# Optimization experiments

Hardware: AMD Instinct MI355X
Metric: run time of the kernel (lower is better)

The kernel has to match this reference:

```python
import jax, jax.numpy as jnp
import numpy as np

CASCADES = 3
D, H, W = 64, 256, 256
HID = 8  # BasicBlock hidden channels


def fdiff(x, axis):
    """Forward difference D x along `axis` (last entry 0) == sparse dx/dy/dz matmul."""
    axis = axis % x.ndim
    pad = [(0, 0)] * x.ndim
    pad[axis] = (0, 1)
    return jnp.pad(jnp.diff(x, axis=axis), pad)


def fdiff_t(y, axis):
    """Exact transpose D^T y of fdiff: (D^T y)_0=-y_0, (D^T y)_j=y_{j-1}-y_j, (D^T y)_{n-1}=y_{n-2}."""
    axis = axis % y.ndim
    n = y.shape[axis]
    yl = jax.lax.slice_in_dim(y, 0, n - 1, axis=axis)  # y[0..n-2]
    pf = [(0, 0)] * y.ndim; pf[axis] = (1, 0)
    pb = [(0, 0)] * y.ndim; pb[axis] = (0, 1)
    return jnp.pad(yl, pf) - jnp.pad(yl, pb)


def conv3d(x, w, b):
    out = jax.lax.conv_general_dilated(
        x, w, window_strides=(1, 1, 1), padding='SAME',
        dimension_numbers=('NCDHW', 'OIDHW', 'NCDHW'))
    return out + b[None, :, None, None, None]


def basic_block(x, w1, b1, w2, b2):
    h = jax.nn.relu(conv3d(x, w1, b1))
    return conv3d(h, w2, b2), jnp.mean(jnp.abs(h))


def ite(t, sino):
    """BeijingGeometry stand-in: one SIRT-style step A^T(sino - A t)/D, A = sum over depth."""
    proj = jnp.sum(t, axis=2)               # [B,1,H,W]
    res = sino - proj
    return jnp.broadcast_to(res[:, :, None], t.shape) / t.shape[2]


def setup_inputs() -> dict:
    key = jax.random.key(0)
    ks = jax.random.split(key, 8)
    image = jax.random.normal(ks[0], (1, 1, D, H, W), dtype=jnp.float32)
    sino = jax.random.normal(ks[1], (1, 1, H, W), dtype=jnp.float32)
    # 4 BasicBlocks stacked on leading axis
    W1 = jax.random.normal(ks[2], (4, HID, 1, 3, 3, 3), dtype=jnp.float32) * 0.1
    B1 = jnp.zeros((4, HID), dtype=jnp.float32)
    W2 = jax.random.normal(ks[3], (4, 1, HID, 3, 3, 3), dtype=jnp.float32) * 0.1
    B2 = jnp.zeros((4, 1), dtype=jnp.float32)
    ntx = jnp.full((CASCADES,), -0.01, dtype=jnp.float32)
    nty = jnp.full((CASCADES,), -0.01, dtype=jnp.float32)
    ntz = jnp.full((CASCADES,), -0.01, dtype=jnp.float32)
    nt = jnp.full((CASCADES,), -0.1, dtype=jnp.float32)
    return {"image": image, "sino": sino, "W1": W1, "B1": B1, "W2": W2, "B2": B2,
            "ntx": ntx, "nty": nty, "ntz": ntz, "nt": nt}


def reference(image, sino, W1, B1, W2, B2, ntx, nty, ntz, nt):
    t = image
    p = q = s = jnp.float32(0.0)
    outs = [image]
    for c in range(CASCADES):
        z = t + ite(t, sino)
        pnew, _ = basic_block(fdiff(z, -1), W1[0], B1[0], W2[0], B2[0])  # d/dx (W axis)
        qnew, _ = basic_block(fdiff(z, -2), W1[1], B1[1], W2[1], B2[1])  # d/dy (H axis)
        snew, _ = basic_block(fdiff(z, -3), W1[2], B1[2], W2[2], B2[2])  # d/dz (D axis)
        znew, _ = basic_block(z, W1[3], B1[3], W2[3], B2[3])
        p = p + ntx[c] * (p - pnew)
        q = q + nty[c] * (q - qnew)
        s = s + ntz[c] * (s - snew)
        z_ = t + nt[c] * (t - znew)
        t = fdiff_t(p, -1) + fdiff_t(q, -2) + fdiff_t(s, -3) + z_
        outs.append(t)
    return jnp.stack(outs, axis=0)  # [cascades+1, B, 1, D, H, W]
```

## Files before the change

kernel.cpp:

```cpp
#include <hip/hip_runtime.h>

#define DD 64
#define HH 256
#define WW 256
#define HW (HH * WW)
#define NVOX (DD * HW)

#define TS 32
#define DR 36
#define HR 34
#define HP 34
#define CHB 22

__global__ __launch_bounds__(256) void k_corr(const float* __restrict__ t,
                                              const float* __restrict__ sino,
                                              float* __restrict__ corr) {
  int idx = blockIdx.x * 256 + threadIdx.x;
  float s = 0.f;
#pragma unroll 8
  for (int d = 0; d < DD; ++d) s += t[d * HW + idx];
  corr[idx] = (sino[idx] - s) * (1.0f / DD);
}

__global__ __launch_bounds__(256, 3) void k_blocks(
    const float* __restrict__ t, const float* __restrict__ corr,
    float* __restrict__ p, float* __restrict__ q, float* __restrict__ s_,
    float* __restrict__ zb,
    const float* __restrict__ W1g, const float* __restrict__ B1g,
    const float* __restrict__ W2g, const float* __restrict__ B2g,
    const float* __restrict__ ntx, const float* __restrict__ nty,
    const float* __restrict__ ntz, const float* __restrict__ nt, int c) {
  __shared__ __align__(16) float dbuf[3][DR][DR];
  __shared__ __align__(16) float hbuf[8][HR][HP];

  const int b = blockIdx.z & 3;
  const int D0 = (blockIdx.z >> 2) * CHB;
  const int Dend = (D0 + CHB < DD) ? (D0 + CHB) : DD;
  const int ty0 = blockIdx.y * TS;
  const int tx0 = blockIdx.x * TS;
  const int tid = threadIdx.x;

  const float* w1 = W1g + b * 216;
  const float* w2 = W2g + b * 216;
  const float b2 = B2g[b];
  const float coef = (b == 0) ? ntx[c] : (b == 1) ? nty[c] : (b == 2) ? ntz[c] : nt[c];
  const float* prevBuf = (b == 0) ? p : (b == 1) ? q : (b == 2) ? s_ : t;
  float* outBuf = (b == 0) ? p : (b == 1) ? q : (b == 2) ? s_ : zb;
  const bool zeroPrev = (c == 0) && (b < 3);

  auto dslot = [](int f) { return (f + 6) % 3; };

  auto load_deriv = [&](int f) {
    int sl = dslot(f);
    for (int i = tid; i < DR * DR; i += 256) {
      int iy = i / DR, ix = i - iy * DR;
      int gy = ty0 - 2 + iy, gx = tx0 - 2 + ix;
      float v = 0.f;
      if (f >= 0 && f < DD && (unsigned)gy < HH && (unsigned)gx < WW) {
        int base = f * HW + gy * WW + gx;
        int cb = gy * WW + gx;
        if (b == 0) {
          if (gx + 1 < WW) v = t[base + 1] - t[base] + corr[cb + 1] - corr[cb];
        } else if (b == 1) {
          if (gy + 1 < HH) v = t[base + WW] - t[base] + corr[cb + WW] - corr[cb];
        } else if (b == 2) {
          if (f + 1 < DD) v = t[base + HW] - t[base];
        } else {
          v = t[base] + corr[cb];
        }
      }
      dbuf[sl][iy][ix] = v;
    }
  };

  auto comp_hidden = [&](int e) {
    const float* d0 = &dbuf[dslot(e - 1)][0][0];
    const float* d1 = &dbuf[dslot(e)][0][0];
    const float* d2 = &dbuf[dslot(e + 1)][0][0];
    for (int pi = tid; pi < 17 * 17; pi += 256) {
      int pr = pi / 17, pc = pi - pr * 17;
      int jy = pr * 2, jx = pc * 2;
      float win[3][4][4];
#pragma unroll
      for (int r = 0; r < 4; ++r) {
        int off = (jy + r) * DR + jx;
        const float2* r0 = (const float2*)(d0 + off);
        const float2* r1 = (const float2*)(d1 + off);
        const float2* r2 = (const float2*)(d2 + off);
        float2 a, bb;
        a = r0[0]; bb = r0[1];
        win[0][r][0] = a.x; win[0][r][1] = a.y; win[0][r][2] = bb.x; win[0][r][3] = bb.y;
        a = r1[0]; bb = r1[1];
        win[1][r][0] = a.x; win[1][r][1] = a.y; win[1][r][2] = bb.x; win[1][r][3] = bb.y;
        a = r2[0]; bb = r2[1];
        win[2][r][0] = a.x; win[2][r][1] = a.y; win[2][r][2] = bb.x; win[2][r][3] = bb.y;
      }
      int gy0 = ty0 - 1 + jy, gx0 = tx0 - 1 + jx;
      bool in00 = ((unsigned)gy0 < HH) && ((unsigned)gx0 < WW);
      bool in01 = ((unsigned)gy0 < HH) && ((unsigned)(gx0 + 1) < WW);
      bool in10 = ((unsigned)(gy0 + 1) < HH) && ((unsigned)gx0 < WW);
      bool in11 = ((unsigned)(gy0 + 1) < HH) && ((unsigned)(gx0 + 1) < WW);
#pragma unroll 2
      for (int ch = 0; ch < 8; ++ch) {
        float bia = B1g[b * 8 + ch];
        float a00 = bia, a01 = bia, a10 = bia, a11 = bia;
        const float* wch = w1 + ch * 27;
#pragma unroll
        for (int kz = 0; kz < 3; ++kz)
#pragma unroll
          for (int ky = 0; ky < 3; ++ky)
#pragma unroll
            for (int kx = 0; kx < 3; ++kx) {
              float wv = wch[kz * 9 + ky * 3 + kx];
              a00 = fmaf(wv, win[kz][ky][kx], a00);
              a01 = fmaf(wv, win[kz][ky][kx + 1], a01);
              a10 = fmaf(wv, win[kz][ky + 1][kx], a10);
              a11 = fmaf(wv, win[kz][ky + 1][kx + 1], a11);
            }
        float2 r0, r1;
        r0.x = in00 ? fmaxf(a00, 0.f) : 0.f;
        r0.y = in01 ? fmaxf(a01, 0.f) : 0.f;
        r1.x = in10 ? fmaxf(a10, 0.f) : 0.f;
        r1.y = in11 ? fmaxf(a11, 0.f) : 0.f;
        *(float2*)&hbuf[ch][jy][jx] = r0;
        *(float2*)&hbuf[ch][jy + 1][jx] = r1;
      }
    }
  };

  const int txi = tid & 15, tyi = tid >> 4;
  const int px0 = txi * 2, py0 = tyi * 2;

  float aM[2][2], aC[2][2], aP[2][2];
#pragma unroll
  for (int i = 0; i < 2; ++i)
#pragma unroll
    for (int j = 0; j < 2; ++j) { aM[i][j] = b2; aC[i][j] = b2; aP[i][j] = b2; }

  load_deriv(D0 - 2);
  load_deriv(D0 - 1);
  load_deriv(D0);
  __syncthreads();

  for (int e = D0 - 1; e <= Dend; ++e) {
    const bool live = (e >= 0 && e < DD);
    if (live) comp_hidden(e);
    __syncthreads();
    if (live) {
#pragma unroll 1
      for (int ch = 0; ch < 8; ++ch) {
        float hwf[4][4];
#pragma unroll
        for (int r = 0; r < 4; ++r) {
          const float2* row = (const float2*)&hbuf[ch][py0 + r][px0];
          float2 a0 = row[0], a1 = row[1];
          hwf[r][0] = a0.x; hwf[r][1] = a0.y; hwf[r][2] = a1.x; hwf[r][3] = a1.y;
        }
        const float* wch = w2 + ch * 27;
#pragma unroll
        for (int ky = 0; ky < 3; ++ky)
#pragma unroll
          for (int kx = 0; kx < 3; ++kx) {
            float w0 = wch[0 + ky * 3 + kx];
            float w1v = wch[9 + ky * 3 + kx];
            float w2v = wch[18 + ky * 3 + kx];
#pragma unroll
            for (int i = 0; i < 2; ++i)
#pragma unroll
              for (int j = 0; j < 2; ++j) {
                float h = hwf[i + ky][j + kx];
                aP[i][j] = fmaf(w0, h, aP[i][j]);
                aC[i][j] = fmaf(w1v, h, aC[i][j]);
                aM[i][j] = fmaf(w2v, h, aM[i][j]);
              }
          }
      }
    }
    if (e >= D0 + 1) {
      int d = e - 1;
#pragma unroll
      for (int i = 0; i < 2; ++i) {
        int gy = ty0 + py0 + i, gx = tx0 + px0;
        size_t v = (size_t)d * HW + gy * WW + gx;
        float2 pr;
        if (zeroPrev) { pr.x = 0.f; pr.y = 0.f; }
        else pr = *(const float2*)&prevBuf[v];
        float2 o;
        o.x = pr.x + coef * (pr.x - aM[i][0]);
        o.y = pr.y + coef * (pr.y - aM[i][1]);
        *(float2*)&outBuf[v] = o;
      }
    }
#pragma unroll
    for (int i = 0; i < 2; ++i)
#pragma unroll
      for (int j = 0; j < 2; ++j) {
        aM[i][j] = aC[i][j]; aC[i][j] = aP[i][j]; aP[i][j] = b2;
      }
    load_deriv(e + 2);
    __syncthreads();
  }
}

__global__ __launch_bounds__(256) void k_combine(
    const float* __restrict__ p, const float* __restrict__ q,
    const float* __restrict__ s_, const float* __restrict__ zb,
    float* __restrict__ tn) {
  int idx = blockIdx.x * 256 + threadIdx.x;
  int x = idx & (WW - 1);
  int y = (idx >> 8) & (HH - 1);
  int d = idx >> 16;
  float v = zb[idx];
  v += (x > 0 ? p[idx - 1] : 0.f) - (x < WW - 1 ? p[idx] : 0.f);
  v += (y > 0 ? q[idx - WW] : 0.f) - (y < HH - 1 ? q[idx] : 0.f);
  v += (d > 0 ? s_[idx - HW] : 0.f) - (d < DD - 1 ? s_[idx] : 0.f);
  tn[idx] = v;
}

extern "C" void kernel_launch(void* const* d_in, const int* in_sizes, int n_in,
                              void* d_out, int out_size, void* d_ws, size_t ws_size,
                              hipStream_t stream) {
  const float* image = (const float*)d_in[0];
  const float* sino  = (const float*)d_in[1];
  const float* W1    = (const float*)d_in[2];
  const float* B1    = (const float*)d_in[3];
  const float* W2    = (const float*)d_in[4];
  const float* B2    = (const float*)d_in[5];
  const float* ntx   = (const float*)d_in[6];
  const float* nty   = (const float*)d_in[7];
  const float* ntz   = (const float*)d_in[8];
  const float* nt    = (const float*)d_in[9];
  float* out = (float*)d_out;

  float* corr = (float*)d_ws;
  float* p  = corr + HW;
  float* q  = p + NVOX;
  float* s_ = q + NVOX;
  float* zb = s_ + NVOX;

  hipMemcpyAsync(out, image, (size_t)NVOX * sizeof(float),
                 hipMemcpyDeviceToDevice, stream);

  for (int c = 0; c < 3; ++c) {
    const float* t = out + (size_t)c * NVOX;
    float* tn = out + (size_t)(c + 1) * NVOX;
    k_corr<<<HW / 256, 256, 0, stream>>>(t, sino, corr);
    k_blocks<<<dim3(WW / TS, HH / TS, 12), 256, 0, stream>>>(
        t, corr, p, q, s_, zb, W1, B1, W2, B2, ntx, nty, ntz, nt, c);
    k_combine<<<NVOX / 256, 256, 0, stream>>>(p, q, s_, zb, tn);
  }
}
```

Measured before the change: 975.6 us.

## Prefetch next depth slice into registers during conv compute and rebalance conv1 work

Global loads for the next depth slice (and the previous-state values needed for the output update) are issued into registers before the conv1/conv2 compute and written to shared memory only afterwards. This hides global memory latency behind the arithmetic. The 289 conv1 patches are redistributed so that the 33 leftover patches are split by channel pairs across 132 threads instead of one thread doing all 8 channels, and the B1 biases are hoisted into registers. The prefetch buffers add about 24 registers per thread, which could hurt occupancy under the launch bound of 3 blocks.

```diff
diff --git a/kernel.cpp b/kernel.cpp
--- a/kernel.cpp
+++ b/kernel.cpp
@@ -11,6 +11,7 @@
 #define HR 34
 #define HP 34
 #define CHB 22
+#define NPF 6
 
 __global__ __launch_bounds__(256) void k_corr(const float* __restrict__ t,
                                               const float* __restrict__ sino,
@@ -42,6 +43,9 @@
 
   const float* w1 = W1g + b * 216;
   const float* w2 = W2g + b * 216;
+  float b1[8];
+#pragma unroll
+  for (int ch = 0; ch < 8; ++ch) b1[ch] = B1g[b * 8 + ch];
   const float b2 = B2g[b];
   const float coef = (b == 0) ? ntx[c] : (b == 1) ? nty[c] : (b == 2) ? ntz[c] : nt[c];
   const float* prevBuf = (b == 0) ? p : (b == 1) ? q : (b == 2) ? s_ : t;
@@ -50,26 +54,94 @@
 
   auto dslot = [](int f) { return (f + 6) % 3; };
 
-  auto load_deriv = [&](int f) {
-    int sl = dslot(f);
-    for (int i = tid; i < DR * DR; i += 256) {
-      int iy = i / DR, ix = i - iy * DR;
-      int gy = ty0 - 2 + iy, gx = tx0 - 2 + ix;
-      float v = 0.f;
-      if (f >= 0 && f < DD && (unsigned)gy < HH && (unsigned)gx < WW) {
-        int base = f * HW + gy * WW + gx;
-        int cb = gy * WW + gx;
-        if (b == 0) {
-          if (gx + 1 < WW) v = t[base + 1] - t[base] + corr[cb + 1] - corr[cb];
-        } else if (b == 1) {
-          if (gy + 1 < HH) v = t[base + WW] - t[base] + corr[cb + WW] - corr[cb];
-        } else if (b == 2) {
-          if (f + 1 < DD) v = t[base + HW] - t[base];
-        } else {
-          v = t[base] + corr[cb];
+  float pA0[NPF], pA1[NPF], pC0[NPF], pC1[NPF];
+
+  auto issue_loads = [&](int f) {
+#pragma unroll
+    for (int k = 0; k < NPF; ++k) {
+      int i = tid + k * 256;
+      pA0[k] = 0.f; pA1[k] = 0.f; pC0[k] = 0.f; pC1[k] = 0.f;
+      if (i < DR * DR) {
+        int iy = i / DR, ix = i - iy * DR;
+        int gy = ty0 - 2 + iy, gx = tx0 - 2 + ix;
+        if (f >= 0 && f < DD && (unsigned)gy < HH && (unsigned)gx < WW) {
+          int base = f * HW + gy * WW + gx;
+          int cb = gy * WW + gx;
+          if (b == 0) {
+            if (gx + 1 < WW) { pA0[k] = t[base]; pA1[k] = t[base + 1];
+                               pC0[k] = corr[cb]; pC1[k] = corr[cb + 1]; }
+          } else if (b == 1) {
+            if (gy + 1 < HH) { pA0[k] = t[base]; pA1[k] = t[base + WW];
+                               pC0[k] = corr[cb]; pC1[k] = corr[cb + WW]; }
+          } else if (b == 2) {
+            if (f + 1 < DD) { pA0[k] = t[base]; pA1[k] = t[base + HW]; }
+          } else {
+            pA0[k] = t[base]; pC0[k] = corr[cb];
+          }
         }
       }
-      dbuf[sl][iy][ix] = v;
+    }
+  };
+  auto write_deriv = [&](int f) {
+    float* dst = &dbuf[dslot(f)][0][0];
+#pragma unroll
+    for (int k = 0; k < NPF; ++k) {
+      int i = tid + k * 256;
+      if (i < DR * DR) {
+        float v;
+        if (b == 3) v = pA0[k] + pC0[k];
+        else v = (pA1[k] - pA0[k]) + (pC1[k] - pC0[k]);
+        dst[i] = v;
+      }
+    }
+  };
+
+  auto conv1_patch = [&](const float* d0, const float* d1, const float* d2,
+                         int jy, int jx, int ch0, int ch1) {
+    float win[3][4][4];
+#pragma unroll
+    for (int r = 0; r < 4; ++r) {
+      int off = (jy + r) * DR + jx;
+      const float2* r0 = (const float2*)(d0 + off);
+      const float2* r1 = (const float2*)(d1 + off);
+      const float2* r2 = (const float2*)(d2 + off);
+      float2 a, bb;
+      a = r0[0]; bb = r0[1];
+      win[0][r][0] = a.x; win[0][r][1] = a.y; win[0][r][2] = bb.x; win[0][r][3] = bb.y;
+      a = r1[0]; bb = r1[1];
+      win[1][r][0] = a.x; win[1][r][1] = a.y; win[1][r][2] = bb.x; win[1][r][3] = bb.y;
+      a = r2[0]; bb = r2[1];
+      win[2][r][0] = a.x; win[2][r][1] = a.y; win[2][r][2] = bb.x; win[2][r][3] = bb.y;
+    }
+    int gy0 = ty0 - 1 + jy, gx0 = tx0 - 1 + jx;
+    bool in00 = ((unsigned)gy0 < HH) && ((unsigned)gx0 < WW);
+    bool in01 = ((unsigned)gy0 < HH) && ((unsigned)(gx0 + 1) < WW);
+    bool in10 = ((unsigned)(gy0 + 1) < HH) && ((unsigned)gx0 < WW);
+    bool in11 = ((unsigned)(gy0 + 1) < HH) && ((unsigned)(gx0 + 1) < WW);
+#pragma unroll 2
+    for (int ch = ch0; ch < ch1; ++ch) {
+      float bia = b1[ch];
+      float a00 = bia, a01 = bia, a10 = bia, a11 = bia;
+      const float* wch = w1 + ch * 27;
+#pragma unroll
+      for (int kz = 0; kz < 3; ++kz)
+#pragma unroll
+        for (int ky = 0; ky < 3; ++ky)
+#pragma unroll
+          for (int kx = 0; kx < 3; ++kx) {
+            float wv = wch[kz * 9 + ky * 3 + kx];
+            a00 = fmaf(wv, win[kz][ky][kx], a00);
+            a01 = fmaf(wv, win[kz][ky][kx + 1], a01);
+            a10 = fmaf(wv, win[kz][ky + 1][kx], a10);
+            a11 = fmaf(wv, win[kz][ky + 1][kx + 1], a11);
+          }
+      float2 r0v, r1v;
+      r0v.x = in00 ? fmaxf(a00, 0.f) : 0.f;
+      r0v.y = in01 ? fmaxf(a01, 0.f) : 0.f;
+      r1v.x = in10 ? fmaxf(a10, 0.f) : 0.f;
+      r1v.y = in11 ? fmaxf(a11, 0.f) : 0.f;
+      *(float2*)&hbuf[ch][jy][jx] = r0v;
+      *(float2*)&hbuf[ch][jy + 1][jx] = r1v;
     }
   };
 
@@ -77,54 +149,15 @@
     const float* d0 = &dbuf[dslot(e - 1)][0][0];
     const float* d1 = &dbuf[dslot(e)][0][0];
     const float* d2 = &dbuf[dslot(e + 1)][0][0];
-    for (int pi = tid; pi < 17 * 17; pi += 256) {
-      int pr = pi / 17, pc = pi - pr * 17;
-      int jy = pr * 2, jx = pc * 2;
-      float win[3][4][4];
-#pragma unroll
-      for (int r = 0; r < 4; ++r) {
-        int off = (jy + r) * DR + jx;
-        const float2* r0 = (const float2*)(d0 + off);
-        const float2* r1 = (const float2*)(d1 + off);
-        const float2* r2 = (const float2*)(d2 + off);
-        float2 a, bb;
-        a = r0[0]; bb = r0[1];
-        win[0][r][0] = a.x; win[0][r][1] = a.y; win[0][r][2] = bb.x; win[0][r][3] = bb.y;
-        a = r1[0]; bb = r1[1];
-        win[1][r][0] = a.x; win[1][r][1] = a.y; win[1][r][2] = bb.x; win[1][r][3] = bb.y;
-        a = r2[0]; bb = r2[1];
-        win[2][r][0] = a.x; win[2][r][1] = a.y; win[2][r][2] = bb.x; win[2][r][3] = bb.y;
-      }
-      int gy0 = ty0 - 1 + jy, gx0 = tx0 - 1 + jx;
-      bool in00 = ((unsigned)gy0 < HH) && ((unsigned)gx0 < WW);
-      bool in01 = ((unsigned)gy0 < HH) && ((unsigned)(gx0 + 1) < WW);
-      bool in10 = ((unsigned)(gy0 + 1) < HH) && ((unsigned)gx0 < WW);
-      bool in11 = ((unsigned)(gy0 + 1) < HH) && ((unsigned)(gx0 + 1) < WW);
-#pragma unroll 2
-      for (int ch = 0; ch < 8; ++ch) {
-        float bia = B1g[b * 8 + ch];
-        float a00 = bia, a01 = bia, a10 = bia, a11 = bia;
-        const float* wch = w1 + ch * 27;
-#pragma unroll
-        for (int kz = 0; kz < 3; ++kz)
-#pragma unroll
-          for (int ky = 0; ky < 3; ++ky)
-#pragma unroll
-            for (int kx = 0; kx < 3; ++kx) {
-              float wv = wch[kz * 9 + ky * 3 + kx];
-              a00 = fmaf(wv, win[kz][ky][kx], a00);
-              a01 = fmaf(wv, win[kz][ky][kx + 1], a01);
-              a10 = fmaf(wv, win[kz][ky + 1][kx], a10);
-              a11 = fmaf(wv, win[kz][ky + 1][kx + 1], a11);
-            }
-        float2 r0, r1;
-        r0.x = in00 ? fmaxf(a00, 0.f) : 0.f;
-        r0.y = in01 ? fmaxf(a01, 0.f) : 0.f;
-        r1.x = in10 ? fmaxf(a10, 0.f) : 0.f;
-        r1.y = in11 ? fmaxf(a11, 0.f) : 0.f;
-        *(float2*)&hbuf[ch][jy][jx] = r0;
-        *(float2*)&hbuf[ch][jy + 1][jx] = r1;
-      }
+    {
+      int prr = tid / 17, pcc = tid - prr * 17;
+      conv1_patch(d0, d1, d2, prr * 2, pcc * 2, 0, 8);
+    }
+    if (tid < 132) {
+      int m = tid >> 2, chp = (tid & 3) << 1;
+      int pi = 256 + m;
+      int prr = pi / 17, pcc = pi - prr * 17;
+      conv1_patch(d0, d1, d2, prr * 2, pcc * 2, chp, chp + 2);
     }
   };
 
@@ -137,13 +170,23 @@
 #pragma unroll
     for (int j = 0; j < 2; ++j) { aM[i][j] = b2; aC[i][j] = b2; aP[i][j] = b2; }
 
-  load_deriv(D0 - 2);
-  load_deriv(D0 - 1);
-  load_deriv(D0);
+  issue_loads(D0 - 2); write_deriv(D0 - 2);
+  issue_loads(D0 - 1); write_deriv(D0 - 1);
+  issue_loads(D0);     write_deriv(D0);
   __syncthreads();
 
   for (int e = D0 - 1; e <= Dend; ++e) {
     const bool live = (e >= 0 && e < DD);
+    issue_loads(e + 2);
+    float2 pr0, pr1;
+    pr0.x = pr0.y = pr1.x = pr1.y = 0.f;
+    const int d = e - 1;
+    const bool doStore = (e >= D0 + 1);
+    if (doStore && !zeroPrev) {
+      size_t v0 = (size_t)d * HW + (size_t)(ty0 + py0) * WW + tx0 + px0;
+      pr0 = *(const float2*)&prevBuf[v0];
+      pr1 = *(const float2*)&prevBuf[v0 + WW];
+    }
     if (live) comp_hidden(e);
     __syncthreads();
     if (live) {
@@ -176,20 +219,16 @@
           }
       }
     }
-    if (e >= D0 + 1) {
-      int d = e - 1;
-#pragma unroll
-      for (int i = 0; i < 2; ++i) {
-        int gy = ty0 + py0 + i, gx = tx0 + px0;
-        size_t v = (size_t)d * HW + gy * WW + gx;
-        float2 pr;
-        if (zeroPrev) { pr.x = 0.f; pr.y = 0.f; }
-        else pr = *(const float2*)&prevBuf[v];
-        float2 o;
-        o.x = pr.x + coef * (pr.x - aM[i][0]);
-        o.y = pr.y + coef * (pr.y - aM[i][1]);
-        *(float2*)&outBuf[v] = o;
-      }
+    write_deriv(e + 2);
+    if (doStore) {
+      size_t v0 = (size_t)d * HW + (size_t)(ty0 + py0) * WW + tx0 + px0;
+      float2 o0, o1;
+      o0.x = pr0.x + coef * (pr0.x - aM[0][0]);
+      o0.y = pr0.y + coef * (pr0.y - aM[0][1]);
+      o1.x = pr1.x + coef * (pr1.x - aM[1][0]);
+      o1.y = pr1.y + coef * (pr1.y - aM[1][1]);
+      *(float2*)&outBuf[v0] = o0;
+      *(float2*)&outBuf[v0 + WW] = o1;
     }
 #pragma unroll
     for (int i = 0; i < 2; ++i)
@@ -197,7 +236,6 @@
       for (int j = 0; j < 2; ++j) {
         aM[i][j] = aC[i][j]; aC[i][j] = aP[i][j]; aP[i][j] = b2;
       }
-    load_deriv(e + 2);
     __syncthreads();
   }
 }
```

Result: no change. 959.7 us (-1.6%).
